# Kernel optimization log

Measured on AMD Instinct MI355X. Metric: run time of the kernel, lower is better.

## Reference

```python
import jax, jax.numpy as jnp
import numpy as np

N_HEAD = 12

def setup_inputs() -> dict:
    key = jax.random.key(0)
    k1, k2, k3, k4, k5 = jax.random.split(key, 5)
    B, T, C = 2, 2048, 768
    x = jax.random.normal(k1, (B, T, C), dtype=jnp.float32)
    W_attn = jax.random.normal(k2, (C, 3 * C), dtype=jnp.float32) * 0.02
    b_attn = jax.random.normal(k3, (3 * C,), dtype=jnp.float32) * 0.02
    W_proj = jax.random.normal(k4, (C, C), dtype=jnp.float32) * 0.02
    b_proj = jax.random.normal(k5, (C,), dtype=jnp.float32) * 0.02
    return {"x": x, "W_attn": W_attn, "b_attn": b_attn, "W_proj": W_proj, "b_proj": b_proj}

def reference(x, W_attn, b_attn, W_proj, b_proj):
    B, T, C = x.shape
    H = N_HEAD
    hd = C // H
    qkv = x @ W_attn + b_attn  # [B,T,3C]
    q, k, v = jnp.split(qkv, 3, axis=2)
    # [B,H,T,hd]
    q = q.reshape(B, T, H, hd).transpose(0, 2, 1, 3)
    k = k.reshape(B, T, H, hd).transpose(0, 2, 1, 3)
    v = v.reshape(B, T, H, hd).transpose(0, 2, 1, 3)
    att = jnp.einsum('bhqd,bhkd->bhqk', q, k) / jnp.sqrt(jnp.float32(hd))
    causal = jnp.tril(jnp.ones((T, T), dtype=bool))
    att = jnp.where(causal[None, None], att, -jnp.inf)
    att = jax.nn.softmax(att, axis=-1)
    y = jnp.einsum('bhqk,bhkd->bhqd', att, v)  # [B,H,T,hd]
    y = y.transpose(0, 2, 1, 3).reshape(B, T, C)
    return y @ W_proj + b_proj
```

## Files before the change

kernel.cpp:

```cpp
#include <hip/hip_runtime.h>
#include <stdint.h>

typedef unsigned short u16;
typedef __attribute__((ext_vector_type(8))) short bf16x8;
typedef __attribute__((ext_vector_type(4))) float f32x4;

__device__ __forceinline__ u16 f2bf(float f){
  union { float f; uint32_t u; } v; v.f = f;
  uint32_t u = v.u;
  u += 0x7FFFu + ((u >> 16) & 1u);
  return (u16)(u >> 16);
}

__device__ __forceinline__ float fexp2(float x){
#if __has_builtin(__builtin_amdgcn_exp2f)
  return __builtin_amdgcn_exp2f(x);
#else
  return exp2f(x);
#endif
}

__device__ __forceinline__ uint32_t cvtpk_bf16(float lo, float hi){
  uint32_t d;
  asm("v_cvt_pk_bf16_f32 %0, %1, %2" : "=v"(d) : "v"(lo), "v"(hi));
  return d;
}

__device__ __forceinline__ f32x4 mfma_bf16(bf16x8 a, bf16x8 b, f32x4 c){
  return __builtin_amdgcn_mfma_f32_16x16x32_bf16(a, b, c, 0, 0, 0);
}

#define GLOADX4(dst, off, sbase)                                            \
  asm volatile("global_load_dwordx4 %0, %1, %2"                             \
               : "=&v"(dst) : "v"(off), "s"(sbase))
#define GLOADX4_O64(dst, off, sbase)                                        \
  asm volatile("global_load_dwordx4 %0, %1, %2 offset:64"                   \
               : "=&v"(dst) : "v"(off), "s"(sbase))

#define QSCALE 0.1803368801111244f

__global__ __launch_bounds__(256) void cast_x_k(const float* __restrict__ x,
                                                u16* __restrict__ xb, int n4){
  int i = blockIdx.x*256 + threadIdx.x;
  if (i >= n4) return;
  float4 v = reinterpret_cast<const float4*>(x)[i];
  uint2 o;
  o.x = (uint32_t)f2bf(v.x) | ((uint32_t)f2bf(v.y) << 16);
  o.y = (uint32_t)f2bf(v.z) | ((uint32_t)f2bf(v.w) << 16);
  reinterpret_cast<uint2*>(xb)[i] = o;
}

__global__ __launch_bounds__(256) void transpose_cast_k(const float* __restrict__ in,
                                                        u16* __restrict__ out,
                                                        int R, int C){
  __shared__ u16 tile[64][66];
  int c0 = blockIdx.x*64, r0 = blockIdx.y*64;
  int tc = threadIdx.x & 63, t4 = threadIdx.x >> 6;
  #pragma unroll
  for (int i=0;i<16;i++){ int r = t4 + i*4; tile[r][tc] = f2bf(in[(size_t)(r0+r)*C + c0 + tc]); }
  __syncthreads();
  #pragma unroll
  for (int i=0;i<16;i++){ int cc = t4 + i*4; out[(size_t)(c0+cc)*R + r0 + tc] = tile[tc][cc]; }
}

#define LDP 40

__global__ __launch_bounds__(256) void gemm_bf16_k(
    const u16* __restrict__ A, const u16* __restrict__ Bt,
    int M, int N, int K, const float* __restrict__ bias, int mode,
    u16* __restrict__ qo, u16* __restrict__ ko, u16* __restrict__ vo,
    float* __restrict__ fo)
{
  __shared__ u16 As[128*LDP];
  __shared__ u16 Bs[128*LDP];
  const int m0 = blockIdx.y*128, n0 = blockIdx.x*128;
  const int tid = threadIdx.x, lane = tid & 63, wid = tid >> 6;
  const int lr = lane & 15, lg = lane >> 4;
  const int wr = wid >> 1, wc = wid & 1;
  f32x4 acc[4][4] = {};
  const int nk = K >> 5;
  for (int kk = 0; kk < nk; ++kk){
    #pragma unroll
    for (int s = 0; s < 2; ++s){
      int ci = tid + 256*s;
      int row = ci >> 2, ch = ci & 3;
      *(uint4*)&As[row*LDP + ch*8] = *(const uint4*)&A[(size_t)(m0+row)*K + kk*32 + ch*8];
      *(uint4*)&Bs[row*LDP + ch*8] = *(const uint4*)&Bt[(size_t)(n0+row)*K + kk*32 + ch*8];
    }
    __syncthreads();
    bf16x8 af[4], bfr[4];
    #pragma unroll
    for (int m=0;m<4;m++) af[m] = *(const bf16x8*)&As[(wr*64 + m*16 + lr)*LDP + lg*8];
    #pragma unroll
    for (int n=0;n<4;n++) bfr[n] = *(const bf16x8*)&Bs[(wc*64 + n*16 + lr)*LDP + lg*8];
    #pragma unroll
    for (int m=0;m<4;m++)
      #pragma unroll
      for (int n=0;n<4;n++)
        acc[m][n] = mfma_bf16(af[m], bfr[n], acc[m][n]);
    __syncthreads();
  }
  if (mode == 0){
    #pragma unroll
    for (int m=0;m<4;m++)
      #pragma unroll
      for (int n=0;n<4;n++){
        int gn = n0 + wc*64 + n*16 + lr;
        float bv = bias[gn];
        #pragma unroll
        for (int r=0;r<4;r++){
          int gm = m0 + wr*64 + m*16 + lg*4 + r;
          fo[(size_t)gm*N + gn] = acc[m][n][r] + bv;
        }
      }
  } else {
    int which = n0 / 768;
    u16* dst = (which==0) ? qo : ko;
    float sc = (which==0) ? QSCALE : 1.0f;
    #pragma unroll
    for (int m=0;m<4;m++)
      #pragma unroll
      for (int n=0;n<4;n++){
        int gn = n0 + wc*64 + n*16 + lr;
        float bv = bias[gn];
        int cn = gn - which*768;
        int h = cn >> 6, d = cn & 63;
        int gm0 = m0 + wr*64 + m*16 + lg*4;
        int b = gm0 >> 11, t0 = gm0 & 2047;
        if (which < 2){
          #pragma unroll
          for (int r=0;r<4;r++)
            dst[(size_t)((b*12 + h)*2048 + t0 + r)*64 + d] = f2bf((acc[m][n][r] + bv)*sc);
        } else {
          uint2 o;
          o.x = cvtpk_bf16(acc[m][n][0]+bv, acc[m][n][1]+bv);
          o.y = cvtpk_bf16(acc[m][n][2]+bv, acc[m][n][3]+bv);
          *(uint2*)&vo[((size_t)((b*12 + h)*64 + d))*2048 + t0] = o;
        }
      }
  }
}

__global__ __launch_bounds__(256) void attn_k(
    const u16* __restrict__ qp, const u16* __restrict__ kp,
    const u16* __restrict__ vtp, u16* __restrict__ yp)
{
  __shared__ f32x4 yl[2][16][64];
  __shared__ float ml[2][4][16];
  __shared__ float ll[2][4][16];
  const int i = blockIdx.x;
  const int bh = i % 24;
  const int qb = 63 - (i / 24);
  const int q0 = qb * 32;
  const int q0A = q0, q0B = q0 + 16;
  const int b = bh / 12, h = bh - b*12;
  const size_t base = (size_t)bh * 131072;
  const int tid = threadIdx.x, lane = tid & 63, wid = tid >> 6;
  const int lr = lane & 15, lg = lane >> 4;
  const int qgA = q0A + lr, qgB = q0B + lr;
  const u16* kbase = kp + base;
  const u16* vbase = vtp + base;

  bf16x8 qfA[2], qfB[2];
  #pragma unroll
  for (int kb=0;kb<2;kb++){
    qfA[kb] = *(const bf16x8*)&qp[base + (size_t)qgA*64 + kb*32 + lg*8];
    qfB[kb] = *(const bf16x8*)&qp[base + (size_t)qgB*64 + kb*32 + lg*8];
  }

  f32x4 yA[4] = {}, yB[4] = {};
  float m2A = 8.f, m2B = 8.f, lA = 0.f, lB = 0.f;
  const int nt = (qb >> 1) + 1;

  uint32_t ka0, ka1, ka2, ka3, va0, va1, va2, va3;
  {
    int p0 = ((0)*32 + (lr>>2)*8 + (0)*4 + (lr&3))*64 + lg*8;
    int p1 = ((1)*32 + (lr>>2)*8 + (0)*4 + (lr&3))*64 + lg*8;
    int p2 = ((0)*32 + (lr>>2)*8 + (1)*4 + (lr&3))*64 + lg*8;
    int p3 = ((1)*32 + (lr>>2)*8 + (1)*4 + (lr&3))*64 + lg*8;
    ka0 = (uint32_t)(wid*4096 + p0)*2u;  ka1 = (uint32_t)(wid*4096 + p1)*2u;
    ka2 = (uint32_t)(wid*4096 + p2)*2u;  ka3 = (uint32_t)(wid*4096 + p3)*2u;
    va0 = (uint32_t)((0*16+lr)*2048 + lg*8 + wid*64)*2u;
    va1 = (uint32_t)((1*16+lr)*2048 + lg*8 + wid*64)*2u;
    va2 = (uint32_t)((2*16+lr)*2048 + lg*8 + wid*64)*2u;
    va3 = (uint32_t)((3*16+lr)*2048 + lg*8 + wid*64)*2u;
  }

  for (int t = wid; t < nt; t += 4){
    bf16x8 kf0,kf1,kf2,kf3,kf4,kf5,kf6,kf7, vf0,vf1,vf2,vf3,vf4,vf5,vf6,vf7;
    GLOADX4    (kf0, ka0, kbase);  GLOADX4_O64(kf1, ka0, kbase);
    GLOADX4    (kf2, ka1, kbase);  GLOADX4_O64(kf3, ka1, kbase);
    GLOADX4    (kf4, ka2, kbase);  GLOADX4_O64(kf5, ka2, kbase);
    GLOADX4    (kf6, ka3, kbase);  GLOADX4_O64(kf7, ka3, kbase);
    GLOADX4    (vf0, va0, vbase);  GLOADX4_O64(vf1, va0, vbase);
    GLOADX4    (vf2, va1, vbase);  GLOADX4_O64(vf3, va1, vbase);
    GLOADX4    (vf4, va2, vbase);  GLOADX4_O64(vf5, va2, vbase);
    GLOADX4    (vf6, va3, vbase);  GLOADX4_O64(vf7, va3, vbase);
    ka0 += 32768u; ka1 += 32768u; ka2 += 32768u; ka3 += 32768u;
    va0 += 512u;   va1 += 512u;   va2 += 512u;   va3 += 512u;

    const int k0 = t*64;
    const int nbmin[4] = {0, 32, 4, 36};

    asm volatile("s_waitcnt vmcnt(8)" ::: "memory");
    __builtin_amdgcn_sched_barrier(0);

    uint32_t pkA[8], pkB[8];
    float smA, smB;
    auto half_qk = [&](int q0H, int qgH, const bf16x8 (&qfH)[2],
                       float m2H, float &lH, uint32_t (&pkH)[8]) -> float {
      f32x4 s[4] = {};
      __builtin_amdgcn_s_setprio(1);
      if (k0      <= q0H + 15){ s[0]=mfma_bf16(kf0,qfH[0],s[0]); s[0]=mfma_bf16(kf1,qfH[1],s[0]); }
      if (k0 + 32 <= q0H + 15){ s[1]=mfma_bf16(kf2,qfH[0],s[1]); s[1]=mfma_bf16(kf3,qfH[1],s[1]); }
      if (k0 +  4 <= q0H + 15){ s[2]=mfma_bf16(kf4,qfH[0],s[2]); s[2]=mfma_bf16(kf5,qfH[1],s[2]); }
      if (k0 + 36 <= q0H + 15){ s[3]=mfma_bf16(kf6,qfH[0],s[3]); s[3]=mfma_bf16(kf7,qfH[1],s[3]); }
      __builtin_amdgcn_s_setprio(0);
      if (k0 + 63 > q0H){
        #pragma unroll
        for (int nb=0;nb<4;nb++){
          int kb0 = k0 + (nb&1)*32 + ((nb>>1)&1)*4 + lg*8;
          #pragma unroll
          for (int r=0;r<4;r++)
            if (kb0 + r > qgH) s[nb][r] = -1e30f;
        }
      }
      float smax = -1e30f, lsum = 0.f;
      #pragma unroll
      for (int nb=0;nb<4;nb++){
        if (k0 + nbmin[nb] <= q0H + 15){
          #pragma unroll
          for (int r=0;r<4;r++){
            smax = fmaxf(smax, s[nb][r]);
            float p = fexp2(s[nb][r] - m2H);
            s[nb][r] = p;
            lsum += p;
          }
        } else {
          #pragma unroll
          for (int r=0;r<4;r++) s[nb][r] = 0.f;
        }
      }
      lH += lsum;
      #pragma unroll
      for (int nb=0;nb<4;nb++){
        pkH[nb*2]   = cvtpk_bf16(s[nb][0], s[nb][1]);
        pkH[nb*2+1] = cvtpk_bf16(s[nb][2], s[nb][3]);
      }
      return smax;
    };
    smA = half_qk(q0A, qgA, qfA, m2A, lA, pkA);
    smB = half_qk(q0B, qgB, qfB, m2B, lB, pkB);

    asm volatile("s_waitcnt vmcnt(0)" ::: "memory");
    __builtin_amdgcn_sched_barrier(0);
    __builtin_amdgcn_s_setprio(1);
    {
      union { uint32_t u[4]; bf16x8 v; } pb;
      pb.u[0]=pkA[0]; pb.u[1]=pkA[1]; pb.u[2]=pkA[4]; pb.u[3]=pkA[5];
      yA[0]=mfma_bf16(vf0,pb.v,yA[0]); yA[1]=mfma_bf16(vf2,pb.v,yA[1]);
      yA[2]=mfma_bf16(vf4,pb.v,yA[2]); yA[3]=mfma_bf16(vf6,pb.v,yA[3]);
      pb.u[0]=pkA[2]; pb.u[1]=pkA[3]; pb.u[2]=pkA[6]; pb.u[3]=pkA[7];
      yA[0]=mfma_bf16(vf1,pb.v,yA[0]); yA[1]=mfma_bf16(vf3,pb.v,yA[1]);
      yA[2]=mfma_bf16(vf5,pb.v,yA[2]); yA[3]=mfma_bf16(vf7,pb.v,yA[3]);
      pb.u[0]=pkB[0]; pb.u[1]=pkB[1]; pb.u[2]=pkB[4]; pb.u[3]=pkB[5];
      yB[0]=mfma_bf16(vf0,pb.v,yB[0]); yB[1]=mfma_bf16(vf2,pb.v,yB[1]);
      yB[2]=mfma_bf16(vf4,pb.v,yB[2]); yB[3]=mfma_bf16(vf6,pb.v,yB[3]);
      pb.u[0]=pkB[2]; pb.u[1]=pkB[3]; pb.u[2]=pkB[6]; pb.u[3]=pkB[7];
      yB[0]=mfma_bf16(vf1,pb.v,yB[0]); yB[1]=mfma_bf16(vf3,pb.v,yB[1]);
      yB[2]=mfma_bf16(vf5,pb.v,yB[2]); yB[3]=mfma_bf16(vf7,pb.v,yB[3]);
    }
    __builtin_amdgcn_s_setprio(0);

    float d = fmaxf(smA - m2A, smB - m2B);
    d = fmaxf(d, __shfl_xor(d, 16));
    d = fmaxf(d, __shfl_xor(d, 32));
    if (!__all(d <= 11.5f)){
      float sAr = fmaxf(smA, __shfl_xor(smA,16)); sAr = fmaxf(sAr, __shfl_xor(sAr,32));
      float sBr = fmaxf(smB, __shfl_xor(smB,16)); sBr = fmaxf(sBr, __shfl_xor(sBr,32));
      float mAn = fmaxf(m2A, sAr), mBn = fmaxf(m2B, sBr);
      float aA = fexp2(m2A - mAn), aB = fexp2(m2B - mBn);
      lA *= aA; lB *= aB;
      #pragma unroll
      for (int n=0;n<4;n++){ yA[n] *= aA; yB[n] *= aB; }
      m2A = mAn; m2B = mBn;
    }
  }

  lA += __shfl_xor(lA, 16);  lA += __shfl_xor(lA, 32);
  lB += __shfl_xor(lB, 16);  lB += __shfl_xor(lB, 32);

  #pragma unroll
  for (int n=0;n<4;n++){ yl[0][wid*4+n][lane] = yA[n]; yl[1][wid*4+n][lane] = yB[n]; }
  if (lg == 0){
    ml[0][wid][lr] = m2A; ll[0][wid][lr] = lA;
    ml[1][wid][lr] = m2B; ll[1][wid][lr] = lB;
  }
  __syncthreads();

  #pragma unroll
  for (int hf=0; hf<2; hf++){
    float m0 = ml[hf][0][lr], m1 = ml[hf][1][lr], m2r = ml[hf][2][lr], m3 = ml[hf][3][lr];
    float ms = fmaxf(fmaxf(m0, m1), fmaxf(m2r, m3));
    float a0 = fexp2(m0 - ms), a1 = fexp2(m1 - ms),
          a2 = fexp2(m2r - ms), a3 = fexp2(m3 - ms);
    float Ls = a0*ll[hf][0][lr] + a1*ll[hf][1][lr] + a2*ll[hf][2][lr] + a3*ll[hf][3][lr];
    f32x4 y0 = yl[hf][0*4+wid][lane], y1 = yl[hf][1*4+wid][lane],
          y2 = yl[hf][2*4+wid][lane], y3 = yl[hf][3*4+wid][lane];
    f32x4 ys;
    #pragma unroll
    for (int r=0;r<4;r++) ys[r] = a0*y0[r] + a1*y1[r] + a2*y2[r] + a3*y3[r];
    float inv = 1.0f / Ls;
    uint2 o;
    o.x = cvtpk_bf16(ys[0]*inv, ys[1]*inv);
    o.y = cvtpk_bf16(ys[2]*inv, ys[3]*inv);
    *(uint2*)&yp[(size_t)(b*2048 + q0 + hf*16 + lr)*768 + h*64 + wid*16 + lg*4] = o;
  }
}

extern "C" void kernel_launch(void* const* d_in, const int* in_sizes, int n_in,
                              void* d_out, int out_size, void* d_ws, size_t ws_size,
                              hipStream_t stream)
{
  const float* x  = (const float*)d_in[0];
  const float* Wa = (const float*)d_in[1];
  const float* ba = (const float*)d_in[2];
  const float* Wp = (const float*)d_in[3];
  const float* bp = (const float*)d_in[4];
  float* out = (float*)d_out;
  char* ws = (char*)d_ws;
  u16* xb  = (u16*)(ws + 0);
  u16* wt  = (u16*)(ws + 6291456);
  u16* wpt = (u16*)(ws + 9830400);
  u16* qb  = (u16*)(ws + 11010048);
  u16* kb  = (u16*)(ws + 17301504);
  u16* vtb = (u16*)(ws + 23592960);
  u16* yb  = (u16*)(ws + 29884416);

  cast_x_k<<<3072, 256, 0, stream>>>(x, xb, 786432);
  transpose_cast_k<<<dim3(36,12), 256, 0, stream>>>(Wa, wt, 768, 2304);
  transpose_cast_k<<<dim3(12,12), 256, 0, stream>>>(Wp, wpt, 768, 768);
  gemm_bf16_k<<<dim3(18,32), 256, 0, stream>>>(xb, wt, 4096, 2304, 768, ba, 1,
                                               qb, kb, vtb, nullptr);
  attn_k<<<1536, 256, 0, stream>>>(qb, kb, vtb, yb);
  gemm_bf16_k<<<dim3(6,32), 256, 0, stream>>>(yb, wpt, 4096, 768, 768, bp, 0,
                                              nullptr, nullptr, nullptr, out);
}
```

Before: 128.9 us.

## Pair long and short causal query blocks per workgroup with two-wave KV split

Each workgroup now processes two query blocks, one from the long end and one from the short end of the causal triangle (qb and 63-qb), with each handled by a pair of waves that split the KV tiles between them. The grid shrinks from 1536 to 768 blocks. This balances per-block work across the causal mask so workgroups finish at similar times, and it halves the cross-wave softmax merge to two partials. The cost is half the KV-split parallelism within a query block, so each wave's serial loop is roughly twice as long.

```diff
diff --git a/kernel.cpp b/kernel.cpp
--- a/kernel.cpp
+++ b/kernel.cpp
@@ -145,17 +145,19 @@
     const u16* __restrict__ qp, const u16* __restrict__ kp,
     const u16* __restrict__ vtp, u16* __restrict__ yp)
 {
-  __shared__ f32x4 yl[2][16][64];
-  __shared__ float ml[2][4][16];
-  __shared__ float ll[2][4][16];
+  __shared__ f32x4 yl[2][2][2][4][64];
+  __shared__ float ml[2][2][2][16];
+  __shared__ float ll[2][2][2][16];
   const int i = blockIdx.x;
   const int bh = i % 24;
-  const int qb = 63 - (i / 24);
-  const int q0 = qb * 32;
-  const int q0A = q0, q0B = q0 + 16;
+  const int pr = i / 24;
   const int b = bh / 12, h = bh - b*12;
   const size_t base = (size_t)bh * 131072;
   const int tid = threadIdx.x, lane = tid & 63, wid = tid >> 6;
+  const int wg = wid >> 1, ws = wid & 1;
+  const int qb = (wg == 0) ? (63 - pr) : pr;
+  const int q0 = qb * 32;
+  const int q0A = q0, q0B = q0 + 16;
   const int lr = lane & 15, lg = lane >> 4;
   const int qgA = q0A + lr, qgB = q0B + lr;
   const u16* kbase = kp + base;
@@ -178,15 +180,15 @@
     int p1 = ((1)*32 + (lr>>2)*8 + (0)*4 + (lr&3))*64 + lg*8;
     int p2 = ((0)*32 + (lr>>2)*8 + (1)*4 + (lr&3))*64 + lg*8;
     int p3 = ((1)*32 + (lr>>2)*8 + (1)*4 + (lr&3))*64 + lg*8;
-    ka0 = (uint32_t)(wid*4096 + p0)*2u;  ka1 = (uint32_t)(wid*4096 + p1)*2u;
-    ka2 = (uint32_t)(wid*4096 + p2)*2u;  ka3 = (uint32_t)(wid*4096 + p3)*2u;
-    va0 = (uint32_t)((0*16+lr)*2048 + lg*8 + wid*64)*2u;
-    va1 = (uint32_t)((1*16+lr)*2048 + lg*8 + wid*64)*2u;
-    va2 = (uint32_t)((2*16+lr)*2048 + lg*8 + wid*64)*2u;
-    va3 = (uint32_t)((3*16+lr)*2048 + lg*8 + wid*64)*2u;
-  }
-
-  for (int t = wid; t < nt; t += 4){
+    ka0 = (uint32_t)(ws*4096 + p0)*2u;  ka1 = (uint32_t)(ws*4096 + p1)*2u;
+    ka2 = (uint32_t)(ws*4096 + p2)*2u;  ka3 = (uint32_t)(ws*4096 + p3)*2u;
+    va0 = (uint32_t)((0*16+lr)*2048 + lg*8 + ws*64)*2u;
+    va1 = (uint32_t)((1*16+lr)*2048 + lg*8 + ws*64)*2u;
+    va2 = (uint32_t)((2*16+lr)*2048 + lg*8 + ws*64)*2u;
+    va3 = (uint32_t)((3*16+lr)*2048 + lg*8 + ws*64)*2u;
+  }
+
+  for (int t = ws; t < nt; t += 2){
     bf16x8 kf0,kf1,kf2,kf3,kf4,kf5,kf6,kf7, vf0,vf1,vf2,vf3,vf4,vf5,vf6,vf7;
     GLOADX4    (kf0, ka0, kbase);  GLOADX4_O64(kf1, ka0, kbase);
     GLOADX4    (kf2, ka1, kbase);  GLOADX4_O64(kf3, ka1, kbase);
@@ -196,8 +198,8 @@
     GLOADX4    (vf2, va1, vbase);  GLOADX4_O64(vf3, va1, vbase);
     GLOADX4    (vf4, va2, vbase);  GLOADX4_O64(vf5, va2, vbase);
     GLOADX4    (vf6, va3, vbase);  GLOADX4_O64(vf7, va3, vbase);
-    ka0 += 32768u; ka1 += 32768u; ka2 += 32768u; ka3 += 32768u;
-    va0 += 512u;   va1 += 512u;   va2 += 512u;   va3 += 512u;
+    ka0 += 16384u; ka1 += 16384u; ka2 += 16384u; ka3 += 16384u;
+    va0 += 256u;   va1 += 256u;   va2 += 256u;   va3 += 256u;
 
     const int k0 = t*64;
     const int nbmin[4] = {0, 32, 4, 36};
@@ -291,30 +293,33 @@
   lB += __shfl_xor(lB, 16);  lB += __shfl_xor(lB, 32);
 
   #pragma unroll
-  for (int n=0;n<4;n++){ yl[0][wid*4+n][lane] = yA[n]; yl[1][wid*4+n][lane] = yB[n]; }
+  for (int n=0;n<4;n++){
+    yl[wg][0][ws][n][lane] = yA[n];
+    yl[wg][1][ws][n][lane] = yB[n];
+  }
   if (lg == 0){
-    ml[0][wid][lr] = m2A; ll[0][wid][lr] = lA;
-    ml[1][wid][lr] = m2B; ll[1][wid][lr] = lB;
+    ml[wg][0][ws][lr] = m2A; ll[wg][0][ws][lr] = lA;
+    ml[wg][1][ws][lr] = m2B; ll[wg][1][ws][lr] = lB;
   }
   __syncthreads();
 
-  #pragma unroll
-  for (int hf=0; hf<2; hf++){
-    float m0 = ml[hf][0][lr], m1 = ml[hf][1][lr], m2r = ml[hf][2][lr], m3 = ml[hf][3][lr];
-    float ms = fmaxf(fmaxf(m0, m1), fmaxf(m2r, m3));
-    float a0 = fexp2(m0 - ms), a1 = fexp2(m1 - ms),
-          a2 = fexp2(m2r - ms), a3 = fexp2(m3 - ms);
-    float Ls = a0*ll[hf][0][lr] + a1*ll[hf][1][lr] + a2*ll[hf][2][lr] + a3*ll[hf][3][lr];
-    f32x4 y0 = yl[hf][0*4+wid][lane], y1 = yl[hf][1*4+wid][lane],
-          y2 = yl[hf][2*4+wid][lane], y3 = yl[hf][3*4+wid][lane];
-    f32x4 ys;
-    #pragma unroll
-    for (int r=0;r<4;r++) ys[r] = a0*y0[r] + a1*y1[r] + a2*y2[r] + a3*y3[r];
+  {
+    float m0 = ml[wg][ws][0][lr], m1 = ml[wg][ws][1][lr];
+    float msx = fmaxf(m0, m1);
+    float a0 = fexp2(m0 - msx), a1 = fexp2(m1 - msx);
+    float Ls = a0*ll[wg][ws][0][lr] + a1*ll[wg][ws][1][lr];
     float inv = 1.0f / Ls;
-    uint2 o;
-    o.x = cvtpk_bf16(ys[0]*inv, ys[1]*inv);
-    o.y = cvtpk_bf16(ys[2]*inv, ys[3]*inv);
-    *(uint2*)&yp[(size_t)(b*2048 + q0 + hf*16 + lr)*768 + h*64 + wid*16 + lg*4] = o;
+    #pragma unroll
+    for (int n=0;n<4;n++){
+      f32x4 y0 = yl[wg][ws][0][n][lane], y1 = yl[wg][ws][1][n][lane];
+      f32x4 ys;
+      #pragma unroll
+      for (int r=0;r<4;r++) ys[r] = a0*y0[r] + a1*y1[r];
+      uint2 o;
+      o.x = cvtpk_bf16(ys[0]*inv, ys[1]*inv);
+      o.y = cvtpk_bf16(ys[2]*inv, ys[3]*inv);
+      *(uint2*)&yp[(size_t)(b*2048 + q0 + ws*16 + lr)*768 + h*64 + n*16 + lg*4] = o;
+    }
   }
 }
 
@@ -342,7 +347,7 @@
   transpose_cast_k<<<dim3(12,12), 256, 0, stream>>>(Wp, wpt, 768, 768);
   gemm_bf16_k<<<dim3(18,32), 256, 0, stream>>>(xb, wt, 4096, 2304, 768, ba, 1,
                                                qb, kb, vtb, nullptr);
-  attn_k<<<1536, 256, 0, stream>>>(qb, kb, vtb, yb);
+  attn_k<<<768, 256, 0, stream>>>(qb, kb, vtb, yb);
   gemm_bf16_k<<<dim3(6,32), 256, 0, stream>>>(yb, wpt, 4096, 768, 768, bp, 0,
                                               nullptr, nullptr, nullptr, out);
 }
```

After: 128.6 us. No clear change (-0.2%).
